# Kernel optimization log

Hardware: AMD Instinct MI355X
Metric: run time of the kernel (lower is better)

## Reference

```python
import jax, jax.numpy as jnp
import numpy as np

NUM_BINS = 256


def _rgb_to_yuv(rgb):  # [B,3,H,W]
    r, g, b = rgb[:, 0], rgb[:, 1], rgb[:, 2]
    y = 0.299 * r + 0.587 * g + 0.114 * b
    u = -0.147 * r - 0.289 * g + 0.436 * b
    v = 0.615 * r - 0.515 * g - 0.100 * b
    return jnp.stack([y, u, v], axis=1)


def _yuv_to_rgb(yuv):  # [B,3,H,W]
    y, u, v = yuv[:, 0], yuv[:, 1], yuv[:, 2]
    r = y + 1.14 * v
    g = y - 0.396 * u - 0.581 * v
    b = y + 2.029 * u
    return jnp.stack([r, g, b], axis=1)


def _equalize_channel(ch):
    # ch: [H, W] in [0, 1]; replicates kornia/TF equalize on one channel.
    im = ch * 255.0
    flat = im.reshape(-1)
    # histc(bins=256, min=0, max=255): bin width 255/256
    bin_idx = jnp.clip(jnp.floor(flat * (NUM_BINS / 255.0)).astype(jnp.int32), 0, NUM_BINS - 1)
    histo = jax.ops.segment_sum(jnp.ones_like(flat), bin_idx, num_segments=NUM_BINS)
    # last nonzero histogram value
    nz = histo > 0
    last_idx = (NUM_BINS - 1) - jnp.argmax(nz[::-1])
    last_val = histo[last_idx]
    step = jnp.floor((jnp.sum(histo) - last_val) / 255.0)  # integer floor-div semantics
    safe_step = jnp.maximum(step, 1.0)
    lut = jnp.floor((jnp.cumsum(histo) + jnp.floor(step / 2.0)) / safe_step)
    lut = jnp.concatenate([jnp.zeros((1,), lut.dtype), lut[:-1]])
    lut = jnp.clip(lut, 0.0, 255.0)
    gather_idx = jnp.clip(flat.astype(jnp.int32), 0, NUM_BINS - 1)
    mapped = jnp.take(lut, gather_idx)
    out = jnp.where(step == 0.0, flat, mapped)
    return (out / 255.0).reshape(ch.shape)


def setup_inputs() -> dict:
    key = jax.random.key(0)
    img = jax.random.uniform(key, (16, 3, 1024, 1024), dtype=jnp.float32)
    return {"img": img}


def reference(img) -> jnp.ndarray:
    img = jnp.clip(img, 0.0, 1.0)
    yuv = _rgb_to_yuv(img)
    y_eq = jax.vmap(_equalize_channel)(yuv[:, 0])  # [B,H,W]
    yuv = jnp.concatenate([y_eq[:, None], yuv[:, 1:]], axis=1)
    return _yuv_to_rgb(yuv)
```

## Files before the change

kernel.cpp:

```cpp
#include <hip/hip_runtime.h>

#define NPIX   (1024*1024)
#define NBATCH 16
#define NBINS  256
#define NSUB   4
#define SUBST  257
#define BPB    128

typedef float v4f __attribute__((ext_vector_type(4)));

__device__ __forceinline__ float clamp01(float x) {
    return fminf(fmaxf(x, 0.0f), 1.0f);
}

__global__ void __launch_bounds__(256)
hist_kernel(const float* __restrict__ img, unsigned int* __restrict__ hist) {
    const int b = blockIdx.y;
    __shared__ unsigned int lh[NSUB * SUBST];
    for (int k = threadIdx.x; k < NSUB * SUBST; k += 256) lh[k] = 0u;
    __syncthreads();

    const int sub = (threadIdx.x & (NSUB - 1)) * SUBST;

    const float* base = img + (size_t)b * 3 * NPIX;
    const v4f* r4 = (const v4f*)(base);
    const v4f* g4 = (const v4f*)(base + NPIX);
    const v4f* b4 = (const v4f*)(base + 2 * NPIX);

    const int n4 = NPIX / 4;
    const int stride = gridDim.x * blockDim.x;
    for (int i = blockIdx.x * blockDim.x + threadIdx.x; i < n4; i += stride) {
        v4f rv = r4[i], gv = g4[i], bv = b4[i];
#pragma unroll
        for (int k = 0; k < 4; ++k) {
            float r = clamp01(rv[k]);
            float g = clamp01(gv[k]);
            float bl = clamp01(bv[k]);
            float y = 0.299f * r + 0.587f * g + 0.114f * bl;
            float flat = y * 255.0f;
            int bin = (int)floorf(flat * (256.0f / 255.0f));
            bin = bin < 0 ? 0 : (bin > NBINS - 1 ? NBINS - 1 : bin);
            atomicAdd(&lh[sub + bin], 1u);
        }
    }
    __syncthreads();
    {
        const int t = threadIdx.x;
        unsigned int s = lh[0 * SUBST + t] + lh[1 * SUBST + t] +
                         lh[2 * SUBST + t] + lh[3 * SUBST + t];
        atomicAdd(&hist[b * NBINS + t], s);
    }
}

__global__ void __launch_bounds__(256)
lut_kernel(const unsigned int* __restrict__ hist,
           float* __restrict__ lut, float* __restrict__ stepflag) {
    const int b = blockIdx.x;
    const int i = threadIdx.x;
    __shared__ float sc[NBINS];
    __shared__ int   li[NBINS];

    float hv = (float)hist[b * NBINS + i];
    sc[i] = hv;
    li[i] = (hv > 0.0f) ? i : -1;
    __syncthreads();

#pragma unroll
    for (int off = 1; off < NBINS; off <<= 1) {
        float v = (i >= off) ? sc[i - off] : 0.0f;
        __syncthreads();
        sc[i] += v;
        __syncthreads();
    }
#pragma unroll
    for (int off = NBINS / 2; off > 0; off >>= 1) {
        int v = (i < off) ? li[i + off] : -1;
        __syncthreads();
        if (i < off && v > li[i]) li[i] = v;
        __syncthreads();
    }

    const float total = sc[NBINS - 1];
    int last = li[0];
    if (last < 0) last = NBINS - 1;
    const float hlast = sc[last] - (last > 0 ? sc[last - 1] : 0.0f);

    const float step = floorf((total - hlast) / 255.0f);
    const float half = floorf(step * 0.5f);
    const float safe = fmaxf(step, 1.0f);

    float l = (i == 0) ? 0.0f : floorf((sc[i - 1] + half) / safe);
    l = fminf(fmaxf(l, 0.0f), 255.0f);
    lut[b * NBINS + i] = l;
    if (i == 0) stepflag[b] = step;
}

__global__ void __launch_bounds__(256)
apply_kernel(const float* __restrict__ img, float* __restrict__ out,
             const float* __restrict__ lut, const float* __restrict__ stepflag) {
    const int b = blockIdx.y;
    __shared__ float llut[NBINS];
    if (threadIdx.x < NBINS) llut[threadIdx.x] = lut[b * NBINS + threadIdx.x];
    __syncthreads();

    const float step = stepflag[b];
    const bool identity = (step == 0.0f);

    const float* base  = img + (size_t)b * 3 * NPIX;
    float*       obase = out + (size_t)b * 3 * NPIX;
    const v4f* r4 = (const v4f*)(base);
    const v4f* g4 = (const v4f*)(base + NPIX);
    const v4f* b4 = (const v4f*)(base + 2 * NPIX);
    v4f* ro = (v4f*)(obase);
    v4f* go = (v4f*)(obase + NPIX);
    v4f* bo = (v4f*)(obase + 2 * NPIX);

    const int n4 = NPIX / 4;
    const int stride = gridDim.x * blockDim.x;
    for (int i = blockIdx.x * blockDim.x + threadIdx.x; i < n4; i += stride) {
        v4f rv = r4[i], gv = g4[i], bv = b4[i];
        v4f orr, org, orb;
#pragma unroll
        for (int k = 0; k < 4; ++k) {
            float r = clamp01(rv[k]);
            float g = clamp01(gv[k]);
            float bl = clamp01(bv[k]);
            float y = 0.299f * r + 0.587f * g + 0.114f * bl;
            float u = -0.147f * r - 0.289f * g + 0.436f * bl;
            float v = 0.615f * r - 0.515f * g - 0.1f * bl;

            float flat = y * 255.0f;
            int gi = (int)flat;
            gi = gi > NBINS - 1 ? NBINS - 1 : gi;
            float ye = identity ? flat : llut[gi];
            ye = ye * (1.0f / 255.0f);

            orr[k] = ye + 1.14f * v;
            org[k] = ye - 0.396f * u - 0.581f * v;
            orb[k] = ye + 2.029f * u;
        }
        __builtin_nontemporal_store(orr, &ro[i]);
        __builtin_nontemporal_store(org, &go[i]);
        __builtin_nontemporal_store(orb, &bo[i]);
    }
}

extern "C" void kernel_launch(void* const* d_in, const int* in_sizes, int n_in,
                              void* d_out, int out_size, void* d_ws, size_t ws_size,
                              hipStream_t stream) {
    const float* img = (const float*)d_in[0];
    float* out = (float*)d_out;

    unsigned int* hist = (unsigned int*)d_ws;
    float* lut      = (float*)((char*)d_ws + NBATCH * NBINS * 4);
    float* stepflag = (float*)((char*)d_ws + 2 * NBATCH * NBINS * 4);

    (void)hipMemsetAsync(d_ws, 0, NBATCH * NBINS * sizeof(unsigned int), stream);

    dim3 grid(BPB, NBATCH), block(256);
    hist_kernel<<<grid, block, 0, stream>>>(img, hist);
    lut_kernel<<<NBATCH, NBINS, 0, stream>>>(hist, lut, stepflag);
    apply_kernel<<<grid, block, 0, stream>>>(img, out, lut, stepflag);
}
```

Before: 377.1 us.

## Fuse histogram, LUT and apply into one cooperative kernel with grid syncs

Replaces the memset plus three kernel launches with a single cooperative kernel of 512 blocks that zeroes the histogram, builds per-batch histograms, syncs the grid, computes the LUT redundantly in every block, and then applies the equalization and YUV to RGB conversion. The aim is to remove launch overhead and the intermediate LUT round trip through global memory. It trades this for two grid-wide barriers, redundant LUT scans in every block, and a smaller grid (32 blocks per batch instead of 128), which may reduce memory-level parallelism. The image is still read twice.

```diff
diff --git a/kernel.cpp b/kernel.cpp
--- a/kernel.cpp
+++ b/kernel.cpp
@@ -1,11 +1,15 @@
 #include <hip/hip_runtime.h>
+#include <hip/hip_cooperative_groups.h>
+
+namespace cg = cooperative_groups;
 
 #define NPIX   (1024*1024)
 #define NBATCH 16
 #define NBINS  256
 #define NSUB   4
 #define SUBST  257
-#define BPB    128
+#define BLKPB  32
+#define GRID   (NBATCH*BLKPB)
 
 typedef float v4f __attribute__((ext_vector_type(4)));
 
@@ -13,117 +17,112 @@
     return fminf(fmaxf(x, 0.0f), 1.0f);
 }
 
-__global__ void __launch_bounds__(256)
-hist_kernel(const float* __restrict__ img, unsigned int* __restrict__ hist) {
-    const int b = blockIdx.y;
+__global__ void __launch_bounds__(256, 2)
+fused_kernel(const float* __restrict__ img, float* __restrict__ out,
+             unsigned int* __restrict__ hist) {
+    const int b   = blockIdx.x >> 5;
+    const int blk = blockIdx.x & 31;
+    const int tid = threadIdx.x;
+
     __shared__ unsigned int lh[NSUB * SUBST];
-    for (int k = threadIdx.x; k < NSUB * SUBST; k += 256) lh[k] = 0u;
-    __syncthreads();
+    __shared__ float sc[NBINS];
+    __shared__ int   li[NBINS];
+    __shared__ float llut[NBINS];
+    __shared__ float s_step;
 
-    const int sub = (threadIdx.x & (NSUB - 1)) * SUBST;
+    cg::grid_group grid = cg::this_grid();
 
+    if (blk == 0)
+        __hip_atomic_store(&hist[b * NBINS + tid], 0u,
+                           __ATOMIC_RELAXED, __HIP_MEMORY_SCOPE_AGENT);
+    for (int k = tid; k < NSUB * SUBST; k += 256) lh[k] = 0u;
+
+    grid.sync();
+
+    const int sub = (tid & (NSUB - 1)) * SUBST;
     const float* base = img + (size_t)b * 3 * NPIX;
     const v4f* r4 = (const v4f*)(base);
     const v4f* g4 = (const v4f*)(base + NPIX);
     const v4f* b4 = (const v4f*)(base + 2 * NPIX);
 
     const int n4 = NPIX / 4;
-    const int stride = gridDim.x * blockDim.x;
-    for (int i = blockIdx.x * blockDim.x + threadIdx.x; i < n4; i += stride) {
+    const int stride = BLKPB * 256;
+    for (int i = blk * 256 + tid; i < n4; i += stride) {
         v4f rv = r4[i], gv = g4[i], bv = b4[i];
 #pragma unroll
         for (int k = 0; k < 4; ++k) {
-            float r = clamp01(rv[k]);
-            float g = clamp01(gv[k]);
+            float r  = clamp01(rv[k]);
+            float g  = clamp01(gv[k]);
             float bl = clamp01(bv[k]);
             float y = 0.299f * r + 0.587f * g + 0.114f * bl;
             float flat = y * 255.0f;
             int bin = (int)floorf(flat * (256.0f / 255.0f));
-            bin = bin < 0 ? 0 : (bin > NBINS - 1 ? NBINS - 1 : bin);
+            bin = bin > NBINS - 1 ? NBINS - 1 : bin;
             atomicAdd(&lh[sub + bin], 1u);
         }
     }
     __syncthreads();
     {
-        const int t = threadIdx.x;
-        unsigned int s = lh[0 * SUBST + t] + lh[1 * SUBST + t] +
-                         lh[2 * SUBST + t] + lh[3 * SUBST + t];
-        atomicAdd(&hist[b * NBINS + t], s);
+        unsigned int s = lh[0 * SUBST + tid] + lh[1 * SUBST + tid] +
+                         lh[2 * SUBST + tid] + lh[3 * SUBST + tid];
+        atomicAdd(&hist[b * NBINS + tid], s);
     }
-}
 
-__global__ void __launch_bounds__(256)
-lut_kernel(const unsigned int* __restrict__ hist,
-           float* __restrict__ lut, float* __restrict__ stepflag) {
-    const int b = blockIdx.x;
-    const int i = threadIdx.x;
-    __shared__ float sc[NBINS];
-    __shared__ int   li[NBINS];
+    grid.sync();
 
-    float hv = (float)hist[b * NBINS + i];
-    sc[i] = hv;
-    li[i] = (hv > 0.0f) ? i : -1;
+    float hv = (float)__hip_atomic_load(&hist[b * NBINS + tid],
+                                        __ATOMIC_RELAXED, __HIP_MEMORY_SCOPE_AGENT);
+    sc[tid] = hv;
+    li[tid] = (hv > 0.0f) ? tid : -1;
     __syncthreads();
 
 #pragma unroll
     for (int off = 1; off < NBINS; off <<= 1) {
-        float v = (i >= off) ? sc[i - off] : 0.0f;
+        float v = (tid >= off) ? sc[tid - off] : 0.0f;
         __syncthreads();
-        sc[i] += v;
+        sc[tid] += v;
         __syncthreads();
     }
 #pragma unroll
     for (int off = NBINS / 2; off > 0; off >>= 1) {
-        int v = (i < off) ? li[i + off] : -1;
+        int v = (tid < off) ? li[tid + off] : -1;
         __syncthreads();
-        if (i < off && v > li[i]) li[i] = v;
+        if (tid < off && v > li[tid]) li[tid] = v;
         __syncthreads();
     }
 
-    const float total = sc[NBINS - 1];
-    int last = li[0];
-    if (last < 0) last = NBINS - 1;
-    const float hlast = sc[last] - (last > 0 ? sc[last - 1] : 0.0f);
+    {
+        const float total = sc[NBINS - 1];
+        int last = li[0];
+        if (last < 0) last = NBINS - 1;
+        const float hlast = sc[last] - (last > 0 ? sc[last - 1] : 0.0f);
 
-    const float step = floorf((total - hlast) / 255.0f);
-    const float half = floorf(step * 0.5f);
-    const float safe = fmaxf(step, 1.0f);
+        const float step = floorf((total - hlast) / 255.0f);
+        const float half = floorf(step * 0.5f);
+        const float safe = fmaxf(step, 1.0f);
 
-    float l = (i == 0) ? 0.0f : floorf((sc[i - 1] + half) / safe);
-    l = fminf(fmaxf(l, 0.0f), 255.0f);
-    lut[b * NBINS + i] = l;
-    if (i == 0) stepflag[b] = step;
-}
-
-__global__ void __launch_bounds__(256)
-apply_kernel(const float* __restrict__ img, float* __restrict__ out,
-             const float* __restrict__ lut, const float* __restrict__ stepflag) {
-    const int b = blockIdx.y;
-    __shared__ float llut[NBINS];
-    if (threadIdx.x < NBINS) llut[threadIdx.x] = lut[b * NBINS + threadIdx.x];
+        float l = (tid == 0) ? 0.0f : floorf((sc[tid - 1] + half) / safe);
+        l = fminf(fmaxf(l, 0.0f), 255.0f);
+        llut[tid] = l;
+        if (tid == 0) s_step = step;
+    }
     __syncthreads();
 
-    const float step = stepflag[b];
+    const float step = s_step;
     const bool identity = (step == 0.0f);
 
-    const float* base  = img + (size_t)b * 3 * NPIX;
-    float*       obase = out + (size_t)b * 3 * NPIX;
-    const v4f* r4 = (const v4f*)(base);
-    const v4f* g4 = (const v4f*)(base + NPIX);
-    const v4f* b4 = (const v4f*)(base + 2 * NPIX);
+    float* obase = out + (size_t)b * 3 * NPIX;
     v4f* ro = (v4f*)(obase);
     v4f* go = (v4f*)(obase + NPIX);
     v4f* bo = (v4f*)(obase + 2 * NPIX);
 
-    const int n4 = NPIX / 4;
-    const int stride = gridDim.x * blockDim.x;
-    for (int i = blockIdx.x * blockDim.x + threadIdx.x; i < n4; i += stride) {
+    for (int i = blk * 256 + tid; i < n4; i += stride) {
         v4f rv = r4[i], gv = g4[i], bv = b4[i];
         v4f orr, org, orb;
 #pragma unroll
         for (int k = 0; k < 4; ++k) {
-            float r = clamp01(rv[k]);
-            float g = clamp01(gv[k]);
+            float r  = clamp01(rv[k]);
+            float g  = clamp01(gv[k]);
             float bl = clamp01(bv[k]);
             float y = 0.299f * r + 0.587f * g + 0.114f * bl;
             float u = -0.147f * r - 0.289f * g + 0.436f * bl;
@@ -150,15 +149,10 @@
                               hipStream_t stream) {
     const float* img = (const float*)d_in[0];
     float* out = (float*)d_out;
+    unsigned int* hist = (unsigned int*)d_ws;
 
-    unsigned int* hist = (unsigned int*)d_ws;
-    float* lut      = (float*)((char*)d_ws + NBATCH * NBINS * 4);
-    float* stepflag = (float*)((char*)d_ws + 2 * NBATCH * NBINS * 4);
-
-    (void)hipMemsetAsync(d_ws, 0, NBATCH * NBINS * sizeof(unsigned int), stream);
-
-    dim3 grid(BPB, NBATCH), block(256);
-    hist_kernel<<<grid, block, 0, stream>>>(img, hist);
-    lut_kernel<<<NBATCH, NBINS, 0, stream>>>(hist, lut, stepflag);
-    apply_kernel<<<grid, block, 0, stream>>>(img, out, lut, stepflag);
+    void* args[] = { (void*)&img, (void*)&out, (void*)&hist };
+    (void)hipLaunchCooperativeKernel((const void*)fused_kernel,
+                                     dim3(GRID), dim3(256),
+                                     args, 0, stream);
 }
```

Result: slower. 489.3 us (+29.7%).
